# Optimization experiments

Hardware: AMD Instinct MI355X
Metric: run time of the kernel (lower is better)

The kernel has to match this reference:

```python
import jax, jax.numpy as jnp
import numpy as np

B, I, H = 256, 512, 512

def setup_inputs() -> dict:
    key = jax.random.key(0)
    ks = jax.random.split(key, 12)
    u = lambda k, s: jax.random.uniform(k, s, dtype=jnp.float32)
    inp = {
        'inputs': jax.random.normal(ks[0], (B, I), dtype=jnp.float32),
        'state': jax.random.normal(ks[1], (B, H), dtype=jnp.float32),
        'sensory_mu': u(ks[2], (I, H)) * 0.5 + 0.3,
        'sensory_sigma': u(ks[3], (I, H)) * 5.0 + 3.0,
        'sensory_W': u(ks[4], (I, H)) * 0.99 + 0.01,
        'sensory_erev': (2.0 * jax.random.randint(ks[5], (I, H), 0, 2) - 1.0).astype(jnp.float32),
        'mu': u(ks[6], (H, H)) * 0.5 + 0.3,
        'sigma': u(ks[7], (H, H)) * 5.0 + 3.0,
        'W': u(ks[8], (H, H)) * 0.99 + 0.01,
        'erev': (2.0 * jax.random.randint(ks[9], (H, H), 0, 2) - 1.0).astype(jnp.float32),
        'vleak': u(ks[10], (H,)) * 0.4 - 0.2,
        'gleak': jnp.ones((H,), dtype=jnp.float32),
        'cm': jnp.full((H,), 0.5, dtype=jnp.float32),
    }
    return inp


def reference(inputs, state, sensory_mu, sensory_sigma, sensory_W, sensory_erev,
              mu, sigma, W, erev, vleak, gleak, cm):
    eps = 1e-08
    # sensory synapses: (B, I, H) broadcast
    s_act = jax.nn.sigmoid((inputs[:, :, None] - sensory_mu[None]) * sensory_sigma[None])
    s_w_act = sensory_W * s_act                      # (B, I, H)
    w_num_s = jnp.sum(s_w_act * sensory_erev, axis=1)  # (B, H)
    w_den_s = jnp.sum(s_w_act, axis=1)                 # (B, H)
    # inter-neuron synapses: (B, H, H) broadcast
    i_act = jax.nn.sigmoid((state[:, :, None] - mu[None]) * sigma[None])
    i_w_act = W * i_act                               # (B, H, H)
    w_num_i = jnp.sum(i_w_act * erev, axis=1)         # (B, H)
    w_den_i = jnp.sum(i_w_act, axis=1)                # (B, H)
    w_numerator = w_num_i + w_num_s
    w_denominator = w_den_i + w_den_s
    G_total = gleak + w_denominator
    tau = cm / (G_total + eps)
    numerator = cm * state + gleak * vleak + w_numerator
    denominator = cm + G_total
    v_inf = numerator / (denominator + eps)
    dt = 0.1
    next_state = v_inf + (state - v_inf) * jnp.exp(-dt / (tau + eps))
    return jnp.tanh(next_state)
```

## Files before the change

### kernel.cpp

```cpp
#include <hip/hip_runtime.h>
#include <stdint.h>

constexpr int NB = 256;
constexpr int NH = 512;
constexpr int NTGT = NB * NH;

constexpr int TB    = 8;
constexpr int CHUNK = 32;
constexpr int HBLK  = 256;

__device__ __constant__ const float SC0 =  0.24781886f;
__device__ __constant__ const float SC1 = -0.01739900f;
__device__ __constant__ const float SC2 =  9.68558e-4f;
__device__ __constant__ const float SC3 = -3.09967e-5f;
__device__ __constant__ const float SC4 =  5.03772e-7f;
__device__ __constant__ const float SC5 = -3.21180e-9f;

__device__ __forceinline__ float clamp7(float z) {
#if __has_builtin(__builtin_amdgcn_fmed3f)
    return __builtin_amdgcn_fmed3f(z, -7.0f, 7.0f);
#else
    return fminf(fmaxf(z, -7.0f), 7.0f);
#endif
}

__global__ __launch_bounds__(256, 8) void ltc_accum(
    const float* __restrict__ inputs,
    const float* __restrict__ state,
    const float* __restrict__ smu, const float* __restrict__ ssg,
    const float* __restrict__ sW,  const float* __restrict__ ser,
    const float* __restrict__ imu, const float* __restrict__ isg,
    const float* __restrict__ iW,  const float* __restrict__ ier,
    float2* __restrict__ part,
    int sBits, int CPB)
{
    __shared__ float xs[CHUNK][TB];

    const int bi    = blockIdx.x;
    const int S     = 1 << sBits;
    const int s     = bi & (S - 1);
    const int rest  = bi >> sBits;
    const int btile = rest & 31;
    const int hhalf = rest >> 5;
    const int b0 = btile * TB;
    const int h  = hhalf * HBLK + threadIdx.x;
    const int g0 = s * (CPB * CHUNK);

    float numA[TB], denA[TB];
#pragma unroll
    for (int bb = 0; bb < TB; ++bb) { numA[bb] = 0.f; denA[bb] = 0.f; }
    float sWsum = 0.f, sWesum = 0.f;

    for (int c = 0; c < CPB; ++c) {
        const int g    = g0 + c * CHUNK;
        const bool sens = g < 512;
        const int  r0   = g & 511;

        const float* __restrict__ src = sens ? inputs : state;
        const float* __restrict__ Pmu = sens ? smu : imu;
        const float* __restrict__ Psg = sens ? ssg : isg;
        const float* __restrict__ PW  = sens ? sW  : iW;
        const float* __restrict__ Per = sens ? ser : ier;

        if (c) __syncthreads();
        {
            const int bb = threadIdx.x >> 5, ii = threadIdx.x & 31;
            const float v = src[(b0 + bb) * 512 + r0 + ii];
            xs[ii][bb] = v;
        }
        __syncthreads();

#pragma unroll 2
        for (int ii = 0; ii < CHUNK; ++ii) {
            const int p = (r0 + ii) * NH + h;
            const float a  = Psg[p];
            const float cc = Pmu[p] * a;
            const float W  = PW[p];
            const float We = W * Per[p];
            sWsum  += W;
            sWesum += We;
#pragma unroll
            for (int bb = 0; bb < TB; ++bb) {
                const float z  = __builtin_fmaf(xs[ii][bb], a, -cc);
                const float zc = clamp7(z);
                const float sq = zc * zc;
                float pl = __builtin_fmaf(SC5, sq, SC4);
                pl = __builtin_fmaf(pl, sq, SC3);
                pl = __builtin_fmaf(pl, sq, SC2);
                pl = __builtin_fmaf(pl, sq, SC1);
                pl = __builtin_fmaf(pl, sq, SC0);
                const float gg = zc * pl;
                denA[bb] = __builtin_fmaf(W,  gg, denA[bb]);
                numA[bb] = __builtin_fmaf(We, gg, numA[bb]);
            }
        }
    }

    float2* __restrict__ slice = part + (size_t)s * NTGT;
#pragma unroll
    for (int bb = 0; bb < TB; ++bb) {
        const float den = __builtin_fmaf(0.5f, sWsum,  denA[bb]);
        const float num = __builtin_fmaf(0.5f, sWesum, numA[bb]);
        slice[(b0 + bb) * NH + h] = make_float2(num, den);
    }
}

__global__ __launch_bounds__(256) void ltc_reduce_epilogue(
    const float* __restrict__ state,
    const float* __restrict__ vleak, const float* __restrict__ gleak,
    const float* __restrict__ cm,
    const float2* __restrict__ part, int S,
    float* __restrict__ out)
{
    const int t = blockIdx.x * 256 + threadIdx.x;
    const int h = t & (NH - 1);

    float wnum = 0.f, wden = 0.f;
    for (int s = 0; s < S; ++s) {
        const float2 p = part[(size_t)s * NTGT + t];
        wnum += p.x; wden += p.y;
    }

    const float st = state[t];
    const float gl = gleak[h];
    const float vl = vleak[h];
    const float c  = cm[h];
    const float eps = 1e-8f;
    const float G = gl + wden;
    const float tau = c / (G + eps);
    const float numerator = c * st + gl * vl + wnum;
    const float denominator = c + G;
    const float v_inf = numerator / (denominator + eps);
    const float next = v_inf + (st - v_inf) * expf(-0.1f / (tau + eps));
    out[t] = tanhf(next);
}

extern "C" void kernel_launch(void* const* d_in, const int* in_sizes, int n_in,
                              void* d_out, int out_size, void* d_ws, size_t ws_size,
                              hipStream_t stream) {
    const float* inputs = (const float*)d_in[0];
    const float* state  = (const float*)d_in[1];
    const float* smu    = (const float*)d_in[2];
    const float* ssg    = (const float*)d_in[3];
    const float* sW     = (const float*)d_in[4];
    const float* ser    = (const float*)d_in[5];
    const float* imu    = (const float*)d_in[6];
    const float* isg    = (const float*)d_in[7];
    const float* iW     = (const float*)d_in[8];
    const float* ier    = (const float*)d_in[9];
    const float* vleak  = (const float*)d_in[10];
    const float* gleak  = (const float*)d_in[11];
    const float* cm     = (const float*)d_in[12];

    int sBits;
    if      (ws_size >= 32ull * NTGT * sizeof(float2)) sBits = 5;
    else if (ws_size >= 16ull * NTGT * sizeof(float2)) sBits = 4;
    else                                               sBits = 3;
    const int S   = 1 << sBits;
    const int CPB = 32 / S;

    float2* part = (float2*)d_ws;

    ltc_accum<<<dim3(S * 64), dim3(256), 0, stream>>>(
        inputs, state, smu, ssg, sW, ser, imu, isg, iW, ier, part, sBits, CPB);
    ltc_reduce_epilogue<<<dim3(NTGT / 256), dim3(256), 0, stream>>>(
        state, vleak, gleak, cm, part, S, (float*)d_out);
}
```

Before: 127.2 us.

## Remap threads to batch rows and tile 16 hidden units per block

Each thread now owns one batch row and accumulates 16 hidden units, so every thread in a block reads the same parameter addresses. Those loads become uniform broadcasts, and per-batch inputs are staged in LDS for all 256 batch rows. Previously each thread owned one hidden unit and eight batch rows, with per-lane parameter loads. The 0.5 offset is folded back into the per-element FMA, the partial-sum layout changes to (h, b), and the epilogue is adjusted to match. It also lowers the occupancy hint and drops the 16-split option, trading a larger LDS fill per chunk and more registers for fewer vector memory loads.

New measurement: 146.1 us. 14.9% more time.

```diff
diff --git a/kernel.cpp b/kernel.cpp
--- a/kernel.cpp
+++ b/kernel.cpp
@@ -1,13 +1,14 @@
 #include <hip/hip_runtime.h>
 #include <stdint.h>
 
-constexpr int NB = 256;
-constexpr int NH = 512;
-constexpr int NTGT = NB * NH;
+constexpr int NB    = 256;
+constexpr int NH    = 512;
+constexpr int NROWS = 1024;
+constexpr int NTGT  = NB * NH;
 
-constexpr int TB    = 8;
+constexpr int THB   = 16;
+constexpr int NHT   = NH / THB;
 constexpr int CHUNK = 32;
-constexpr int HBLK  = 256;
 
 __device__ __constant__ const float SC0 =  0.24781886f;
 __device__ __constant__ const float SC1 = -0.01739900f;
@@ -24,7 +25,7 @@
 #endif
 }
 
-__global__ __launch_bounds__(256, 8) void ltc_accum(
+__global__ __launch_bounds__(256, 4) void ltc_accum(
     const float* __restrict__ inputs,
     const float* __restrict__ state,
     const float* __restrict__ smu, const float* __restrict__ ssg,
@@ -32,26 +33,24 @@
     const float* __restrict__ imu, const float* __restrict__ isg,
     const float* __restrict__ iW,  const float* __restrict__ ier,
     float2* __restrict__ part,
-    int sBits, int CPB)
+    int sBits)
 {
-    __shared__ float xs[CHUNK][TB];
-
+    __shared__ float xs[CHUNK][NB + 1];
     const int bi    = blockIdx.x;
     const int S     = 1 << sBits;
     const int s     = bi & (S - 1);
-    const int rest  = bi >> sBits;
-    const int btile = rest & 31;
-    const int hhalf = rest >> 5;
-    const int b0 = btile * TB;
-    const int h  = hhalf * HBLK + threadIdx.x;
-    const int g0 = s * (CPB * CHUNK);
+    const int htile = bi >> sBits;
+    const int h0    = htile * THB;
+    const int rowsPerBlock = NROWS >> sBits;
+    const int nchunk = rowsPerBlock / CHUNK;
+    const int g0    = s * rowsPerBlock;
+    const int b     = threadIdx.x;
 
-    float numA[TB], denA[TB];
+    float accN[THB], accD[THB];
 #pragma unroll
-    for (int bb = 0; bb < TB; ++bb) { numA[bb] = 0.f; denA[bb] = 0.f; }
-    float sWsum = 0.f, sWesum = 0.f;
+    for (int hh = 0; hh < THB; ++hh) { accN[hh] = 0.f; accD[hh] = 0.f; }
 
-    for (int c = 0; c < CPB; ++c) {
+    for (int c = 0; c < nchunk; ++c) {
         const int g    = g0 + c * CHUNK;
         const bool sens = g < 512;
         const int  r0   = g & 511;
@@ -63,25 +62,25 @@
         const float* __restrict__ Per = sens ? ser : ier;
 
         if (c) __syncthreads();
-        {
-            const int bb = threadIdx.x >> 5, ii = threadIdx.x & 31;
-            const float v = src[(b0 + bb) * 512 + r0 + ii];
-            xs[ii][bb] = v;
+#pragma unroll 4
+        for (int k = 0; k < CHUNK; ++k) {
+            const int lin = k * 256 + threadIdx.x;
+            const int ii  = lin & (CHUNK - 1);
+            const int bb  = lin >> 5;
+            xs[ii][bb] = src[bb * 512 + r0 + ii];
         }
         __syncthreads();
 
-#pragma unroll 2
         for (int ii = 0; ii < CHUNK; ++ii) {
-            const int p = (r0 + ii) * NH + h;
-            const float a  = Psg[p];
-            const float cc = Pmu[p] * a;
-            const float W  = PW[p];
-            const float We = W * Per[p];
-            sWsum  += W;
-            sWesum += We;
+            const float xv = xs[ii][b];
+            const int prow = (r0 + ii) * NH + h0;
 #pragma unroll
-            for (int bb = 0; bb < TB; ++bb) {
-                const float z  = __builtin_fmaf(xs[ii][bb], a, -cc);
+            for (int hh = 0; hh < THB; ++hh) {
+                const float a  = Psg[prow + hh];
+                const float cc = Pmu[prow + hh] * a;
+                const float W  = PW [prow + hh];
+                const float We = W * Per[prow + hh];
+                const float z  = __builtin_fmaf(xv, a, -cc);
                 const float zc = clamp7(z);
                 const float sq = zc * zc;
                 float pl = __builtin_fmaf(SC5, sq, SC4);
@@ -89,19 +88,17 @@
                 pl = __builtin_fmaf(pl, sq, SC2);
                 pl = __builtin_fmaf(pl, sq, SC1);
                 pl = __builtin_fmaf(pl, sq, SC0);
-                const float gg = zc * pl;
-                denA[bb] = __builtin_fmaf(W,  gg, denA[bb]);
-                numA[bb] = __builtin_fmaf(We, gg, numA[bb]);
+                const float sig = __builtin_fmaf(zc, pl, 0.5f);
+                accD[hh] = __builtin_fmaf(W,  sig, accD[hh]);
+                accN[hh] = __builtin_fmaf(We, sig, accN[hh]);
             }
         }
     }
 
     float2* __restrict__ slice = part + (size_t)s * NTGT;
 #pragma unroll
-    for (int bb = 0; bb < TB; ++bb) {
-        const float den = __builtin_fmaf(0.5f, sWsum,  denA[bb]);
-        const float num = __builtin_fmaf(0.5f, sWesum, numA[bb]);
-        slice[(b0 + bb) * NH + h] = make_float2(num, den);
+    for (int hh = 0; hh < THB; ++hh) {
+        slice[(h0 + hh) * NB + b] = make_float2(accN[hh], accD[hh]);
     }
 }
 
@@ -113,7 +110,8 @@
     float* __restrict__ out)
 {
     const int t = blockIdx.x * 256 + threadIdx.x;
-    const int h = t & (NH - 1);
+    const int h = t >> 8;
+    const int b = t & (NB - 1);
 
     float wnum = 0.f, wden = 0.f;
     for (int s = 0; s < S; ++s) {
@@ -121,7 +119,7 @@
         wnum += p.x; wden += p.y;
     }
 
-    const float st = state[t];
+    const float st = state[b * NH + h];
     const float gl = gleak[h];
     const float vl = vleak[h];
     const float c  = cm[h];
@@ -132,7 +130,7 @@
     const float denominator = c + G;
     const float v_inf = numerator / (denominator + eps);
     const float next = v_inf + (st - v_inf) * expf(-0.1f / (tau + eps));
-    out[t] = tanhf(next);
+    out[b * NH + h] = tanhf(next);
 }
 
 extern "C" void kernel_launch(void* const* d_in, const int* in_sizes, int n_in,
@@ -152,17 +150,13 @@
     const float* gleak  = (const float*)d_in[11];
     const float* cm     = (const float*)d_in[12];
 
-    int sBits;
-    if      (ws_size >= 32ull * NTGT * sizeof(float2)) sBits = 5;
-    else if (ws_size >= 16ull * NTGT * sizeof(float2)) sBits = 4;
-    else                                               sBits = 3;
-    const int S   = 1 << sBits;
-    const int CPB = 32 / S;
+    const int sBits = (ws_size >= 32ull * NTGT * sizeof(float2)) ? 5 : 3;
+    const int S     = 1 << sBits;
 
     float2* part = (float2*)d_ws;
 
-    ltc_accum<<<dim3(S * 64), dim3(256), 0, stream>>>(
-        inputs, state, smu, ssg, sW, ser, imu, isg, iW, ier, part, sBits, CPB);
+    ltc_accum<<<dim3(NHT * S), dim3(256), 0, stream>>>(
+        inputs, state, smu, ssg, sW, ser, imu, isg, iW, ier, part, sBits);
     ltc_reduce_epilogue<<<dim3(NTGT / 256), dim3(256), 0, stream>>>(
         state, vleak, gleak, cm, part, S, (float*)d_out);
 }
```
